# Optimization experiments

Hardware: AMD Instinct MI355X
Metric: run time of the kernel (lower is better)

## Reference

```python
import jax, jax.numpy as jnp
import numpy as np
from jax import lax

# LIF neuron parameters (norse LIFParameters defaults)
DT = 0.001
TAU_SYN_INV = 200.0
TAU_MEM_INV = 100.0
V_LEAK = 0.0
V_TH = 1.0
V_RESET = 0.0
ALPHA = 100.0  # SuperSpike surrogate slope


@jax.custom_vjp
def spike(x):
    # heaviside step with SuperSpike surrogate gradient
    return (x > 0).astype(x.dtype)

def _spike_fwd(x):
    return (x > 0).astype(x.dtype), x

def _spike_bwd(x, g):
    sg = 1.0 / (ALPHA * jnp.abs(x) + 1.0) ** 2
    return (g * sg,)

spike.defvjp(_spike_fwd, _spike_bwd)


def setup_inputs() -> dict:
    key = jax.random.key(0)
    T, B, N = 1024, 32, 2048
    input_tensor = jax.random.normal(key, (T, B, N), dtype=jnp.float32)
    return {"input_tensor": input_tensor}


def reference(input_tensor):
    # state_fallback: zero (v, i) shaped like one timestep
    v0 = jnp.zeros_like(input_tensor[0])
    i0 = jnp.zeros_like(input_tensor[0])

    def step(carry, x_t):
        v, i = carry
        # membrane integration: dv = dt * tau_mem_inv * ((v_leak - v) + i)
        v_dec = v + DT * TAU_MEM_INV * ((V_LEAK - v) + i)
        # synaptic current decay: di = -dt * tau_syn_inv * i
        i_dec = i * (1.0 - DT * TAU_SYN_INV)
        # spike + reset
        z = spike(v_dec - V_TH)
        v_new = (1.0 - z) * v_dec + z * V_RESET
        # inject input current
        i_new = i_dec + x_t
        return (v_new, i_new), z

    (v_f, i_f), spikes = lax.scan(step, (v0, i0), input_tensor)
    # matches SNN.forward: (stacked outputs, final state)
    return spikes, v_f, i_f
```

## Files before the change

### kernel.cpp

```cpp
#include <hip/hip_runtime.h>


#define TT 1024
#define BN 65536
#define BN2 (BN / 2)
#define U  32

typedef float v2f __attribute__((ext_vector_type(2)));

__global__ __launch_bounds__(128, 1) void snn_lif_kernel(
    const float* __restrict__ xf,
    float* __restrict__ outf)
{
    const int idx = blockIdx.x * 128 + threadIdx.x;
    const v2f* __restrict__ xp = (const v2f*)xf + idx;
    v2f* __restrict__ sp = (v2f*)outf + idx;

    float v0 = 0.0f, v1 = 0.0f;
    float i0 = 0.0f, i1 = 0.0f;

    const float c_mem = 0.1f;
    const float c_syn = 0.8f;

    auto step = [&](float& v, float& i, float xin) -> float {
        float dv    = __fmul_rn(c_mem, __fadd_rn(__fsub_rn(0.0f, v), i));
        float v_dec = __fadd_rn(v, dv);
        float i_dec = __fmul_rn(i, c_syn);
        bool fired  = (v_dec > 1.0f);
        v = fired ? 0.0f : v_dec;
        i = __fadd_rn(i_dec, xin);
        return fired ? 1.0f : 0.0f;
    };

    v2f xa[U], xb[U];

    #pragma unroll
    for (int k = 0; k < U; ++k)
        xa[k] = __builtin_nontemporal_load(&xp[(size_t)k * BN2]);

    #pragma unroll 1
    for (int t0 = 0; t0 < TT; t0 += 2 * U) {
        #pragma unroll
        for (int k = 0; k < U; ++k)
            xb[k] = __builtin_nontemporal_load(&xp[(size_t)(t0 + U + k) * BN2]);

        #pragma unroll
        for (int k = 0; k < U; ++k) {
            v2f z;
            z.x = step(v0, i0, xa[k].x);
            z.y = step(v1, i1, xa[k].y);
            __builtin_nontemporal_store(z, &sp[(size_t)(t0 + k) * BN2]);
        }

        if (t0 + 2 * U < TT) {
            #pragma unroll
            for (int k = 0; k < U; ++k)
                xa[k] = __builtin_nontemporal_load(&xp[(size_t)(t0 + 2 * U + k) * BN2]);
        }

        #pragma unroll
        for (int k = 0; k < U; ++k) {
            v2f z;
            z.x = step(v0, i0, xb[k].x);
            z.y = step(v1, i1, xb[k].y);
            __builtin_nontemporal_store(z, &sp[(size_t)(t0 + U + k) * BN2]);
        }
    }

    v2f* vf = (v2f*)(outf + (size_t)TT * BN) + idx;
    v2f* iff = (v2f*)(outf + (size_t)TT * BN + BN) + idx;
    v2f vfin; vfin.x = v0; vfin.y = v1;
    v2f ifin; ifin.x = i0; ifin.y = i1;
    *vf = vfin;
    *iff = ifin;
}

extern "C" void kernel_launch(void* const* d_in, const int* in_sizes, int n_in,
                              void* d_out, int out_size, void* d_ws, size_t ws_size,
                              hipStream_t stream) {
    const float* x = (const float*)d_in[0];
    float* out = (float*)d_out;
    snn_lif_kernel<<<BN2 / 128, 128, 0, stream>>>(x, out);
}
```

Baseline: 414.7 us.

## Split compute and store roles across warps with LDS double-buffered spike slab

Blocks grow to 256 threads. The first 128 threads load inputs and run the serial LIF recurrence, writing spikes into a double-buffered shared-memory slab. The other 128 threads drain the slab to global memory with nontemporal stores, synchronised by block barriers each phase. The intent is to take store issue off the latency-bound recurrence warps, at the cost of LDS traffic and barrier stalls that couple the two roles.

```diff
diff --git a/kernel.cpp b/kernel.cpp
--- a/kernel.cpp
+++ b/kernel.cpp
@@ -5,74 +5,117 @@
 #define BN 65536
 #define BN2 (BN / 2)
 #define U  32
+#define NPH (TT / U)
 
 typedef float v2f __attribute__((ext_vector_type(2)));
 
-__global__ __launch_bounds__(128, 1) void snn_lif_kernel(
+__global__ __launch_bounds__(256, 1) void snn_lif_kernel(
     const float* __restrict__ xf,
     float* __restrict__ outf)
 {
-    const int idx = blockIdx.x * 128 + threadIdx.x;
-    const v2f* __restrict__ xp = (const v2f*)xf + idx;
-    v2f* __restrict__ sp = (v2f*)outf + idx;
+    __shared__ v2f slab[2][U][128];
 
-    float v0 = 0.0f, v1 = 0.0f;
-    float i0 = 0.0f, i1 = 0.0f;
+    const int tid = threadIdx.x;
+    const int lane_idx = blockIdx.x * 128 + (tid & 127);
 
-    const float c_mem = 0.1f;
-    const float c_syn = 0.8f;
+    if (tid < 128) {
+        const v2f* __restrict__ xp = (const v2f*)xf + lane_idx;
 
-    auto step = [&](float& v, float& i, float xin) -> float {
-        float dv    = __fmul_rn(c_mem, __fadd_rn(__fsub_rn(0.0f, v), i));
-        float v_dec = __fadd_rn(v, dv);
-        float i_dec = __fmul_rn(i, c_syn);
-        bool fired  = (v_dec > 1.0f);
-        v = fired ? 0.0f : v_dec;
-        i = __fadd_rn(i_dec, xin);
-        return fired ? 1.0f : 0.0f;
-    };
+        float v0 = 0.0f, v1 = 0.0f;
+        float i0 = 0.0f, i1 = 0.0f;
+        const float c_mem = 0.1f;
+        const float c_syn = 0.8f;
 
-    v2f xa[U], xb[U];
+        auto step = [&](float& v, float& i, float xin) -> float {
+            float dv    = __fmul_rn(c_mem, __fadd_rn(__fsub_rn(0.0f, v), i));
+            float v_dec = __fadd_rn(v, dv);
+            float i_dec = __fmul_rn(i, c_syn);
+            bool fired  = (v_dec > 1.0f);
+            v = fired ? 0.0f : v_dec;
+            i = __fadd_rn(i_dec, xin);
+            return fired ? 1.0f : 0.0f;
+        };
 
-    #pragma unroll
-    for (int k = 0; k < U; ++k)
-        xa[k] = __builtin_nontemporal_load(&xp[(size_t)k * BN2]);
-
-    #pragma unroll 1
-    for (int t0 = 0; t0 < TT; t0 += 2 * U) {
+        v2f xa[U], xb[U];
         #pragma unroll
         for (int k = 0; k < U; ++k)
-            xb[k] = __builtin_nontemporal_load(&xp[(size_t)(t0 + U + k) * BN2]);
+            xa[k] = __builtin_nontemporal_load(&xp[(size_t)k * BN2]);
+        #pragma unroll
+        for (int k = 0; k < U; ++k)
+            xb[k] = __builtin_nontemporal_load(&xp[(size_t)(U + k) * BN2]);
 
+        #pragma unroll 1
+        for (int p = 0; p < NPH; p += 2) {
+            #pragma unroll
+            for (int k = 0; k < U; ++k) {
+                v2f z;
+                z.x = step(v0, i0, xa[k].x);
+                z.y = step(v1, i1, xa[k].y);
+                slab[0][k][tid] = z;
+            }
+            if (p + 2 < NPH) {
+                #pragma unroll
+                for (int k = 0; k < U; ++k)
+                    xa[k] = __builtin_nontemporal_load(
+                        &xp[(size_t)((p + 2) * U + k) * BN2]);
+            }
+            asm volatile("s_waitcnt lgkmcnt(0)" ::: "memory");
+            __builtin_amdgcn_s_barrier();
+
+            #pragma unroll
+            for (int k = 0; k < U; ++k) {
+                v2f z;
+                z.x = step(v0, i0, xb[k].x);
+                z.y = step(v1, i1, xb[k].y);
+                slab[1][k][tid] = z;
+            }
+            if (p + 3 < NPH) {
+                #pragma unroll
+                for (int k = 0; k < U; ++k)
+                    xb[k] = __builtin_nontemporal_load(
+                        &xp[(size_t)((p + 3) * U + k) * BN2]);
+            }
+            asm volatile("s_waitcnt lgkmcnt(0)" ::: "memory");
+            __builtin_amdgcn_s_barrier();
+        }
+
+        v2f* vf  = (v2f*)(outf + (size_t)TT * BN) + lane_idx;
+        v2f* iff = (v2f*)(outf + (size_t)TT * BN + BN) + lane_idx;
+        v2f a; a.x = v0; a.y = v1; *vf = a;
+        v2f b; b.x = i0; b.y = i1; *iff = b;
+    } else {
+        v2f* __restrict__ sp = (v2f*)outf + lane_idx;
+        const int wtid = tid - 128;
+
+        #pragma unroll 1
+        for (int p = 0; p < NPH; p += 2) {
+            if (p > 0) {
+                #pragma unroll
+                for (int k = 0; k < U; ++k) {
+                    v2f z = slab[1][k][wtid];
+                    __builtin_nontemporal_store(
+                        z, &sp[(size_t)((p - 1) * U + k) * BN2]);
+                }
+            }
+            asm volatile("s_waitcnt lgkmcnt(0)" ::: "memory");
+            __builtin_amdgcn_s_barrier();
+
+            #pragma unroll
+            for (int k = 0; k < U; ++k) {
+                v2f z = slab[0][k][wtid];
+                __builtin_nontemporal_store(
+                    z, &sp[(size_t)(p * U + k) * BN2]);
+            }
+            asm volatile("s_waitcnt lgkmcnt(0)" ::: "memory");
+            __builtin_amdgcn_s_barrier();
+        }
         #pragma unroll
         for (int k = 0; k < U; ++k) {
-            v2f z;
-            z.x = step(v0, i0, xa[k].x);
-            z.y = step(v1, i1, xa[k].y);
-            __builtin_nontemporal_store(z, &sp[(size_t)(t0 + k) * BN2]);
-        }
-
-        if (t0 + 2 * U < TT) {
-            #pragma unroll
-            for (int k = 0; k < U; ++k)
-                xa[k] = __builtin_nontemporal_load(&xp[(size_t)(t0 + 2 * U + k) * BN2]);
-        }
-
-        #pragma unroll
-        for (int k = 0; k < U; ++k) {
-            v2f z;
-            z.x = step(v0, i0, xb[k].x);
-            z.y = step(v1, i1, xb[k].y);
-            __builtin_nontemporal_store(z, &sp[(size_t)(t0 + U + k) * BN2]);
+            v2f z = slab[1][k][wtid];
+            __builtin_nontemporal_store(
+                z, &sp[(size_t)((NPH - 1) * U + k) * BN2]);
         }
     }
-
-    v2f* vf = (v2f*)(outf + (size_t)TT * BN) + idx;
-    v2f* iff = (v2f*)(outf + (size_t)TT * BN + BN) + idx;
-    v2f vfin; vfin.x = v0; vfin.y = v1;
-    v2f ifin; ifin.x = i0; ifin.y = i1;
-    *vf = vfin;
-    *iff = ifin;
 }
 
 extern "C" void kernel_launch(void* const* d_in, const int* in_sizes, int n_in,
@@ -80,5 +123,5 @@
                               hipStream_t stream) {
     const float* x = (const float*)d_in[0];
     float* out = (float*)d_out;
-    snn_lif_kernel<<<BN2 / 128, 128, 0, stream>>>(x, out);
+    snn_lif_kernel<<<BN2 / 128, 256, 0, stream>>>(x, out);
 }
```

After: 417.7 us. Within noise of the previous version (+0.7%).

## Stream inputs through an LDS ring buffer via async global-to-LDS loads

Applied to the files above, without the earlier changes.

Replaces the register double-buffered nontemporal loads with asynchronous global_load_lds DMA into a per-wave LDS ring, keeping a prefetch distance of 16 timesteps and using manual vmcnt waits. The aim is to free the registers that held 64 buffered inputs and to keep memory requests continuously in flight, instead of issuing them in bursts. In exchange it relies on hand-tuned waitcnt counts that interact with the output stores, which risks ordering hazards or stalls. Each timestep now also pays an LDS read.

```diff
diff --git a/kernel.cpp b/kernel.cpp
--- a/kernel.cpp
+++ b/kernel.cpp
@@ -4,21 +4,28 @@
 #define TT 1024
 #define BN 65536
 #define BN2 (BN / 2)
-#define U  32
+#define D  16
+#define RS 32
 
 typedef float v2f __attribute__((ext_vector_type(2)));
+typedef __attribute__((address_space(3))) float* lds_fp;
+typedef const __attribute__((address_space(1))) float* glb_fp;
 
 __global__ __launch_bounds__(128, 1) void snn_lif_kernel(
     const float* __restrict__ xf,
     float* __restrict__ outf)
 {
-    const int idx = blockIdx.x * 128 + threadIdx.x;
-    const v2f* __restrict__ xp = (const v2f*)xf + idx;
+    __shared__ float ring[2][RS][128];
+
+    const int tid  = threadIdx.x;
+    const int lane = tid & 63;
+    const int wid  = tid >> 6;
+    const int idx  = blockIdx.x * 128 + tid;
+
+    const float* gw = xf + (size_t)blockIdx.x * 256 + wid * 128 + lane;
     v2f* __restrict__ sp = (v2f*)outf + idx;
 
-    float v0 = 0.0f, v1 = 0.0f;
-    float i0 = 0.0f, i1 = 0.0f;
-
+    float v0 = 0.0f, v1 = 0.0f, i0 = 0.0f, i1 = 0.0f;
     const float c_mem = 0.1f;
     const float c_syn = 0.8f;
 
@@ -32,47 +39,50 @@
         return fired ? 1.0f : 0.0f;
     };
 
-    v2f xa[U], xb[U];
-
     #pragma unroll
-    for (int k = 0; k < U; ++k)
-        xa[k] = __builtin_nontemporal_load(&xp[(size_t)k * BN2]);
+    for (int u = 0; u < D; ++u) {
+        const float* g = gw + (size_t)u * BN;
+        __builtin_amdgcn_global_load_lds((glb_fp)g,
+                                         (lds_fp)&ring[wid][u][0], 4, 0, 0);
+        __builtin_amdgcn_global_load_lds((glb_fp)(g + 64),
+                                         (lds_fp)&ring[wid][u][64], 4, 0, 0);
+    }
+    asm volatile("s_waitcnt vmcnt(0)" ::: "memory");
 
     #pragma unroll 1
-    for (int t0 = 0; t0 < TT; t0 += 2 * U) {
-        #pragma unroll
-        for (int k = 0; k < U; ++k)
-            xb[k] = __builtin_nontemporal_load(&xp[(size_t)(t0 + U + k) * BN2]);
+    for (int u = 0; u < TT - D; ++u) {
+        asm volatile("s_waitcnt vmcnt(46)" ::: "memory");
+        __builtin_amdgcn_sched_barrier(0);
 
-        #pragma unroll
-        for (int k = 0; k < U; ++k) {
-            v2f z;
-            z.x = step(v0, i0, xa[k].x);
-            z.y = step(v1, i1, xa[k].y);
-            __builtin_nontemporal_store(z, &sp[(size_t)(t0 + k) * BN2]);
-        }
+        v2f x = ((v2f*)&ring[wid][u & (RS - 1)][0])[lane];
+        v2f z;
+        z.x = step(v0, i0, x.x);
+        z.y = step(v1, i1, x.y);
 
-        if (t0 + 2 * U < TT) {
-            #pragma unroll
-            for (int k = 0; k < U; ++k)
-                xa[k] = __builtin_nontemporal_load(&xp[(size_t)(t0 + 2 * U + k) * BN2]);
-        }
+        const float* g = gw + (size_t)(u + D) * BN;
+        __builtin_amdgcn_global_load_lds((glb_fp)g,
+                                         (lds_fp)&ring[wid][(u + D) & (RS - 1)][0], 4, 0, 0);
+        __builtin_amdgcn_global_load_lds((glb_fp)(g + 64),
+                                         (lds_fp)&ring[wid][(u + D) & (RS - 1)][64], 4, 0, 0);
 
-        #pragma unroll
-        for (int k = 0; k < U; ++k) {
-            v2f z;
-            z.x = step(v0, i0, xb[k].x);
-            z.y = step(v1, i1, xb[k].y);
-            __builtin_nontemporal_store(z, &sp[(size_t)(t0 + U + k) * BN2]);
-        }
+        __builtin_nontemporal_store(z, &sp[(size_t)u * BN2]);
     }
 
-    v2f* vf = (v2f*)(outf + (size_t)TT * BN) + idx;
+    asm volatile("s_waitcnt vmcnt(0)" ::: "memory");
+
+    #pragma unroll 1
+    for (int u = TT - D; u < TT; ++u) {
+        v2f x = ((v2f*)&ring[wid][u & (RS - 1)][0])[lane];
+        v2f z;
+        z.x = step(v0, i0, x.x);
+        z.y = step(v1, i1, x.y);
+        __builtin_nontemporal_store(z, &sp[(size_t)u * BN2]);
+    }
+
+    v2f* vf  = (v2f*)(outf + (size_t)TT * BN) + idx;
     v2f* iff = (v2f*)(outf + (size_t)TT * BN + BN) + idx;
-    v2f vfin; vfin.x = v0; vfin.y = v1;
-    v2f ifin; ifin.x = i0; ifin.y = i1;
-    *vf = vfin;
-    *iff = ifin;
+    v2f a; a.x = v0; a.y = v1; *vf = a;
+    v2f b; b.x = i0; b.y = i1; *iff = b;
 }
 
 extern "C" void kernel_launch(void* const* d_in, const int* in_sizes, int n_in,
```

Measured after the change: 434.9 us. 4.9% more time.
